# Kernel optimization log

Measured on AMD Instinct MI355X. Metric: run time of the kernel, lower is better.

The kernel has to match this reference:

```python
import jax, jax.numpy as jnp
import numpy as np

B, LH, HF = 65536, 128, 32
VC_MIN = 0.0


def _theta_init():
    # Deterministic parameter init, matching the torch constructor defaults.
    def spinv(x):
        return float(np.log(np.exp(max(x, 1e-4)) - 1.0 + 1e-6))
    vals = [
        0.0,                                  # alpha_raw: log(0.5/(1-0.5))
        float(np.log(np.exp(1.0) - 1.0 + 1e-6)),   # c_raw  (c_init=1.0)
        float(np.log(np.exp(0.1) - 1.0 + 1e-6)),   # kappa_raw (kappa_init=0.1)
        float(np.log(np.exp(0.15) - 1.0 + 1e-6)),  # vc_raw (vc_eff=0.15)
        -6.0,   # log_qx
        -6.0,   # log_qu
        -5.0,   # log_r
        0.0,    # log_q_scale
        -6.0,   # log_p0_xx
        -4.0,   # log_p0_uu
        spinv(0.1),   # a1_raw
        spinv(0.05),  # d1_raw
        spinv(0.5),   # d2_raw
        spinv(0.5),   # d3_raw
        0.0,    # b1
        0.0,    # b2
        0.1,    # beta
        float(np.arctanh(0.9)),  # rho_m_raw
        -4.0,   # log_qm
        -4.0,   # log_p0_mm
    ]
    return np.asarray(vals, dtype=np.float32)


def setup_inputs() -> dict:
    key = jax.random.key(0)
    k1, k2, k3, k4, k5 = jax.random.split(key, 5)
    return {
        "v_hist": jax.random.normal(k1, (B, LH), dtype=jnp.float32),
        "dt_hist": 0.01 + 0.1 * jax.random.uniform(k2, (B, LH), dtype=jnp.float32),
        "x_obs_hist": jax.random.normal(k3, (B, LH), dtype=jnp.float32),
        "v_fut": jax.random.normal(k4, (B, HF), dtype=jnp.float32),
        "dt_fut": 0.01 + 0.1 * jax.random.uniform(k5, (B, HF), dtype=jnp.float32),
        "theta": jnp.asarray(_theta_init()),
    }


def _forward(v_hist, dt_hist, x_obs_hist, v_fut, dt_fut, theta):
    sp = jax.nn.softplus
    alpha = jax.nn.sigmoid(theta[0])
    c = sp(theta[1]); kappa = sp(theta[2]); vc = sp(theta[3]) + VC_MIN
    qx = jnp.exp(theta[4]); qu = jnp.exp(theta[5]); R = jnp.exp(theta[6])
    qs = jnp.exp(theta[7]); p0xx = jnp.exp(theta[8]); p0uu = jnp.exp(theta[9])
    a1 = sp(theta[10]); d1 = sp(theta[11]); d2 = sp(theta[12]); d3 = sp(theta[13])
    b1 = theta[14]; b2 = theta[15]; beta = theta[16]
    rho_m = jnp.tanh(theta[17]); qm = jnp.exp(theta[18]); p0mm = jnp.exp(theta[19])

    Bn, Lh = v_hist.shape
    dtype = v_hist.dtype
    eye = jnp.eye(3, dtype=dtype)

    def predict(s, P, v, dv, dt):
        x, u, m = s[:, 0], s[:, 1], s[:, 2]
        rho = jnp.exp(-alpha * dt)
        forcing = jax.nn.relu(v * v - vc * vc)
        cl = (-a1 * u + b1 * v + b2 * dv
              - d1 * u * u - d2 * u * jnp.abs(v) - d3 * u * jnp.abs(u))
        x_p = x + u * dt
        u_p = rho * u - kappa * x * dt + c * forcing * dt + cl * dt + beta * m
        m_p = rho_m * m
        s_p = jnp.stack([x_p, u_p, m_p], axis=1)
        z = jnp.zeros_like(dt); o = jnp.ones_like(dt)
        Fm = jnp.stack([
            jnp.stack([o, dt, z], axis=1),
            jnp.stack([-kappa * dt, rho, beta * o], axis=1),
            jnp.stack([z, z, rho_m * o], axis=1)], axis=1)  # [B,3,3]
        qdiag = jnp.stack([qs * qx * dt, qs * qu * dt, qm * o], axis=1)  # [B,3]
        P_p = jnp.einsum('bij,bjk,blk->bil', Fm, P, Fm) + qdiag[:, :, None] * eye
        return s_p, P_p

    def update(s, P, y):
        innov = y - s[:, 0]
        S = P[:, 0, 0] + R
        K = P[:, :, 0] / S[:, None]            # [B,3]
        s_u = s + K * innov[:, None]
        IKH = eye - K[:, :, None] * eye[0]     # I - K H, H = [1,0,0]
        P_u = (jnp.einsum('bij,bjk,blk->bil', IKH, P, IKH)
               + R * (K[:, :, None] * K[:, None, :]))
        return s_u, P_u

    s0 = jnp.zeros((Bn, 3), dtype).at[:, 0].set(x_obs_hist[:, 0])
    P0 = jnp.broadcast_to(jnp.diag(jnp.stack([p0xx, p0uu, p0mm])).astype(dtype),
                          (Bn, 3, 3))

    # History steps k = 1 .. Lh-1 (scan over time axis, [T, B] layout)
    v_h = v_hist[:, :Lh - 1].T
    dv_h = jnp.concatenate(
        [jnp.zeros((1, Bn), dtype), (v_hist[:, 1:Lh - 1] - v_hist[:, :Lh - 2]).T], axis=0)
    dt_h = jnp.maximum(dt_hist[:, 1:], 1e-6).T
    y_h = x_obs_hist[:, 1:].T

    def hist_step(carry, inp):
        s, P = carry
        v, dv, dt, y = inp
        s, P = predict(s, P, v, dv, dt)
        s, P = update(s, P, y)
        return (s, P), None

    (s, P), _ = jax.lax.scan(hist_step, (s0, P0), (v_h, dv_h, dt_h, y_h))

    # Future rollout (predict only)
    v_f = v_fut.T
    dv_f = (v_fut - jnp.concatenate([v_hist[:, -1:], v_fut[:, :-1]], axis=1)).T
    dt_f = jnp.maximum(dt_fut, 1e-6).T

    def fut_step(carry, inp):
        s, P = carry
        v, dv, dt = inp
        s, P = predict(s, P, v, dv, dt)
        return (s, P), (s[:, 0], P[:, 0, 0], s[:, 1])

    _, (x_preds, x_vars, u_ests) = jax.lax.scan(fut_step, (s, P), (v_f, dv_f, dt_f))
    return x_preds.T, x_vars.T, u_ests.T  # each [B, Hf]


def reference(v_hist, dt_hist, x_obs_hist, v_fut, dt_fut, theta):
    return _forward(v_hist, dt_hist, x_obs_hist, v_fut, dt_fut, theta)
```

## Files before the change

### kernel.cpp

```cpp
#include <hip/hip_runtime.h>
#include <math.h>

#define BATCH 65536
#define LHIST 128
#define HFUT  32

__device__ __forceinline__ float softplusf(float x) {
    return fmaxf(x, 0.0f) + log1pf(expf(-fabsf(x)));
}

#define KSLOT(buf, st, c, row) ((((((buf)*16 + (st))*3 + (c))*256)) + (row))

__global__ __launch_bounds__(512, 2) void kalman_fwd(
    const float* __restrict__ v_hist,
    const float* __restrict__ dt_hist,
    const float* __restrict__ x_obs,
    const float* __restrict__ v_fut,
    const float* __restrict__ dt_fut,
    const float* __restrict__ theta,
    float* __restrict__ out)
{
    const int tid = threadIdx.x;
    const bool isP = (tid < 256);
    const int row  = tid & 255;
    const int b    = blockIdx.x * 256 + row;

    __shared__ float Kls[2 * 16 * 3 * 256];

    const float alpha = 1.0f / (1.0f + expf(-theta[0]));
    const float c     = softplusf(theta[1]);
    const float kappa = softplusf(theta[2]);
    const float vc    = softplusf(theta[3]);
    const float qx    = expf(theta[4]);
    const float qu    = expf(theta[5]);
    const float Rn    = expf(theta[6]);
    const float qs    = expf(theta[7]);
    const float p0xx  = expf(theta[8]);
    const float p0uu  = expf(theta[9]);
    const float a1    = softplusf(theta[10]);
    const float d1    = softplusf(theta[11]);
    const float d2    = softplusf(theta[12]);
    const float d3    = softplusf(theta[13]);
    const float b1    = theta[14];
    const float b2    = theta[15];
    const float beta  = theta[16];
    const float rho_m = tanhf(theta[17]);
    const float qm    = expf(theta[18]);
    const float p0mm  = expf(theta[19]);
    const float vc2   = vc * vc;
    const float qxs   = qs * qx;
    const float qus   = qs * qu;
    const float rm2   = rho_m * rho_m;
    const float nal2e = -alpha * 1.44269504088896340736f;

    float p00 = p0xx, p01 = 0.0f, p02 = 0.0f, p11 = p0uu, p12 = 0.0f, p22 = p0mm;
    float sx = 0.0f, su = 0.0f, sm = 0.0f, vp1 = 0.0f, vp2 = 0.0f;

    auto P_step = [&](float dt_raw, int buf, int st) {
        float dt  = fmaxf(dt_raw, 1e-6f);
        float rho = __builtin_amdgcn_exp2f(nal2e * dt);
        float kdt = kappa * dt;
        float f0 = p00 + dt * p01;
        float f1 = p01 + dt * p11;
        float f2 = p02 + dt * p12;
        float g0 = -kdt * p00 + rho * p01 + beta * p02;
        float g1 = -kdt * p01 + rho * p11 + beta * p12;
        float g2 = -kdt * p02 + rho * p12 + beta * p22;
        float n00 = f0 + dt * f1 + qxs * dt;
        float n01 = -kdt * f0 + rho * f1 + beta * f2;
        float n02 = rho_m * f2;
        float n11 = -kdt * g0 + rho * g1 + beta * g2 + qus * dt;
        float n12 = rho_m * g2;
        float n22 = rm2 * p22 + qm;
        float S    = n00 + Rn;
        float Sinv = __builtin_amdgcn_rcpf(S);
        float K0 = n00 * Sinv, K1 = n01 * Sinv, K2 = n02 * Sinv;
        Kls[KSLOT(buf, st, 0, row)] = K0;
        Kls[KSLOT(buf, st, 1, row)] = K1;
        Kls[KSLOT(buf, st, 2, row)] = K2;
        float a = 1.0f - K0;
        p00 = a * a * n00 + Rn * K0 * K0;
        p01 = a * (n01 - K1 * n00) + Rn * K0 * K1;
        p02 = a * (n02 - K2 * n00) + Rn * K0 * K2;
        p11 = S * K1 * K1 - 2.0f * K1 * n01 + n11;
        p12 = S * K1 * K2 - K2 * n01 - K1 * n02 + n12;
        p22 = S * K2 * K2 - 2.0f * K2 * n02 + n22;
    };

    auto P_pred = [&](float dt_raw) {
        float dt  = fmaxf(dt_raw, 1e-6f);
        float rho = __builtin_amdgcn_exp2f(nal2e * dt);
        float kdt = kappa * dt;
        float f0 = p00 + dt * p01;
        float f1 = p01 + dt * p11;
        float f2 = p02 + dt * p12;
        float g0 = -kdt * p00 + rho * p01 + beta * p02;
        float g1 = -kdt * p01 + rho * p11 + beta * p12;
        float g2 = -kdt * p02 + rho * p12 + beta * p22;
        float n00 = f0 + dt * f1 + qxs * dt;
        float n01 = -kdt * f0 + rho * f1 + beta * f2;
        float n02 = rho_m * f2;
        float n11 = -kdt * g0 + rho * g1 + beta * g2 + qus * dt;
        float n12 = rho_m * g2;
        float n22 = rm2 * p22 + qm;
        p00 = n00; p01 = n01; p02 = n02; p11 = n11; p12 = n12; p22 = n22;
    };

    auto s_pred = [&](float v, float dv, float dt_raw) {
        float dt  = fmaxf(dt_raw, 1e-6f);
        float rho = __builtin_amdgcn_exp2f(nal2e * dt);
        float forcing = fmaxf(v * v - vc2, 0.0f);
        float cl = -a1 * su + b1 * v + b2 * dv
                 - d1 * su * su - d2 * su * fabsf(v) - d3 * su * fabsf(su);
        float kdt = kappa * dt;
        float x_p = sx + su * dt;
        float u_p = rho * su - kdt * sx + c * forcing * dt + cl * dt + beta * sm;
        float m_p = rho_m * sm;
        sx = x_p; su = u_p; sm = m_p;
    };

    auto s_step = [&](float vnew, float dt_raw, float y, int buf, int st) {
        float K0 = Kls[KSLOT(buf, st, 0, row)];
        float K1 = Kls[KSLOT(buf, st, 1, row)];
        float K2 = Kls[KSLOT(buf, st, 2, row)];
        s_pred(vp1, vp1 - vp2, dt_raw);
        float innov = y - sx;
        sx += K0 * innov; su += K1 * innov; sm += K2 * innov;
        vp2 = vp1; vp1 = vnew;
    };

    const float4* v4 = (const float4*)(v_hist  + (size_t)b * LHIST);
    const float4* d4 = (const float4*)(dt_hist + (size_t)b * LHIST);
    const float4* y4 = (const float4*)(x_obs   + (size_t)b * LHIST);

    {
        if (isP) {
            float cdt[16];
            float4* C = (float4*)cdt;
            #pragma unroll
            for (int i = 0; i < 4; ++i) C[i] = d4[i];
            #pragma unroll
            for (int st = 1; st < 16; ++st) P_step(cdt[st], 0, st);
        }
        __syncthreads();

        #pragma unroll 1
        for (int k = 1; k < 8; ++k) {
            if (isP) {
                float cdt[16];
                float4* C = (float4*)cdt;
                #pragma unroll
                for (int i = 0; i < 4; ++i) C[i] = d4[k * 4 + i];
                int buf = k & 1;
                P_step(cdt[0], buf, 0);
                #pragma unroll
                for (int st = 1; st < 16; ++st) P_step(cdt[st], buf, st);
            } else {
                int j = k - 1;
                float cv[16], cd[16], cy[16];
                float4* V = (float4*)cv; float4* D = (float4*)cd; float4* Y = (float4*)cy;
                #pragma unroll
                for (int i = 0; i < 4; ++i) {
                    V[i] = v4[j * 4 + i]; D[i] = d4[j * 4 + i]; Y[i] = y4[j * 4 + i];
                }
                int buf = j & 1;
                if (j == 0) {
                    sx = cy[0]; vp1 = cv[0]; vp2 = cv[0];
                } else {
                    s_step(cv[0], cd[0], cy[0], buf, 0);
                }
                #pragma unroll
                for (int st = 1; st < 16; ++st) s_step(cv[st], cd[st], cy[st], buf, st);
            }
            __syncthreads();
        }

        if (!isP) {
            const int j = 7;
            float cv[16], cd[16], cy[16];
            float4* V = (float4*)cv; float4* D = (float4*)cd; float4* Y = (float4*)cy;
            #pragma unroll
            for (int i = 0; i < 4; ++i) {
                V[i] = v4[j * 4 + i]; D[i] = d4[j * 4 + i]; Y[i] = y4[j * 4 + i];
            }
            s_step(cv[0], cd[0], cy[0], 1, 0);
            #pragma unroll
            for (int st = 1; st < 16; ++st) s_step(cv[st], cd[st], cy[st], 1, st);
        }
    }

    if (isP) {
        float fdt[32];
        float4* FD = (float4*)fdt;
        const float4* df4 = (const float4*)(dt_fut + (size_t)b * HFUT);
        #pragma unroll
        for (int i = 0; i < 8; ++i) FD[i] = df4[i];
        float oxv[32];
        #pragma unroll
        for (int j = 0; j < HFUT; ++j) { P_pred(fdt[j]); oxv[j] = p00; }
        float4* xv = (float4*)(out + (size_t)BATCH * HFUT + (size_t)b * HFUT);
        float4* OXV = (float4*)oxv;
        #pragma unroll
        for (int i = 0; i < 8; ++i) xv[i] = OXV[i];
    } else {
        float fv[32], fdt[32];
        float4* FV = (float4*)fv; float4* FD = (float4*)fdt;
        const float4* vf4 = (const float4*)(v_fut  + (size_t)b * HFUT);
        const float4* df4 = (const float4*)(dt_fut + (size_t)b * HFUT);
        #pragma unroll
        for (int i = 0; i < 8; ++i) { FV[i] = vf4[i]; FD[i] = df4[i]; }
        float oxp[32], oue[32];
        float vp = vp1;
        #pragma unroll
        for (int j = 0; j < HFUT; ++j) {
            s_pred(fv[j], fv[j] - vp, fdt[j]);
            vp = fv[j];
            oxp[j] = sx; oue[j] = su;
        }
        float4* xp = (float4*)(out + (size_t)b * HFUT);
        float4* ue = (float4*)(out + 2 * (size_t)BATCH * HFUT + (size_t)b * HFUT);
        float4* OXP = (float4*)oxp; float4* OUE = (float4*)oue;
        #pragma unroll
        for (int i = 0; i < 8; ++i) { xp[i] = OXP[i]; ue[i] = OUE[i]; }
    }
}

extern "C" void kernel_launch(void* const* d_in, const int* in_sizes, int n_in,
                              void* d_out, int out_size, void* d_ws, size_t ws_size,
                              hipStream_t stream) {
    const float* v_hist  = (const float*)d_in[0];
    const float* dt_hist = (const float*)d_in[1];
    const float* x_obs   = (const float*)d_in[2];
    const float* v_fut   = (const float*)d_in[3];
    const float* dt_fut  = (const float*)d_in[4];
    const float* theta   = (const float*)d_in[5];
    float* out = (float*)d_out;

    dim3 grid(BATCH / 256), block(512);
    hipLaunchKernelGGL(kalman_fwd, grid, block, 0, stream,
                       v_hist, dt_hist, x_obs, v_fut, dt_fut, theta, out);
}
```

Before: 179.6 us.

## Software-pipeline chunk loads with double-buffered registers across producer/consumer phases

Unrolls the history loop into explicit phases where each warp group prefetches the next 16-step chunk of inputs into a second register buffer while it computes on the current one. This is meant to hide global-memory load latency behind the serial Kalman recurrence instead of stalling at the start of each chunk. The cost is higher register pressure from the doubled input buffers, which under launch_bounds(512,2) could cause spills.

New measurement: 204.3 us. 1.14x slower.

```diff
diff --git a/kernel.cpp b/kernel.cpp
--- a/kernel.cpp
+++ b/kernel.cpp
@@ -9,7 +9,7 @@
     return fmaxf(x, 0.0f) + log1pf(expf(-fabsf(x)));
 }
 
-#define KSLOT(buf, st, c, row) ((((((buf)*16 + (st))*3 + (c))*256)) + (row))
+#define KSLOT(buf, st, c, row) (((((buf)*16 + (st))*3 + (c))*256) + (row))
 
 __global__ __launch_bounds__(512, 2) void kalman_fwd(
     const float* __restrict__ v_hist,
@@ -133,76 +133,96 @@
     const float4* d4 = (const float4*)(dt_hist + (size_t)b * LHIST);
     const float4* y4 = (const float4*)(x_obs   + (size_t)b * LHIST);
 
-    {
-        if (isP) {
-            float cdt[16];
-            float4* C = (float4*)cdt;
-            #pragma unroll
-            for (int i = 0; i < 4; ++i) C[i] = d4[i];
-            #pragma unroll
-            for (int st = 1; st < 16; ++st) P_step(cdt[st], 0, st);
-        }
-        __syncthreads();
-
-        #pragma unroll 1
-        for (int k = 1; k < 8; ++k) {
-            if (isP) {
-                float cdt[16];
-                float4* C = (float4*)cdt;
-                #pragma unroll
-                for (int i = 0; i < 4; ++i) C[i] = d4[k * 4 + i];
-                int buf = k & 1;
-                P_step(cdt[0], buf, 0);
-                #pragma unroll
-                for (int st = 1; st < 16; ++st) P_step(cdt[st], buf, st);
-            } else {
-                int j = k - 1;
-                float cv[16], cd[16], cy[16];
-                float4* V = (float4*)cv; float4* D = (float4*)cd; float4* Y = (float4*)cy;
-                #pragma unroll
-                for (int i = 0; i < 4; ++i) {
-                    V[i] = v4[j * 4 + i]; D[i] = d4[j * 4 + i]; Y[i] = y4[j * 4 + i];
-                }
-                int buf = j & 1;
-                if (j == 0) {
-                    sx = cy[0]; vp1 = cv[0]; vp2 = cv[0];
-                } else {
-                    s_step(cv[0], cd[0], cy[0], buf, 0);
-                }
-                #pragma unroll
-                for (int st = 1; st < 16; ++st) s_step(cv[st], cd[st], cy[st], buf, st);
-            }
-            __syncthreads();
-        }
-
-        if (!isP) {
-            const int j = 7;
-            float cv[16], cd[16], cy[16];
-            float4* V = (float4*)cv; float4* D = (float4*)cd; float4* Y = (float4*)cy;
-            #pragma unroll
-            for (int i = 0; i < 4; ++i) {
-                V[i] = v4[j * 4 + i]; D[i] = d4[j * 4 + i]; Y[i] = y4[j * 4 + i];
-            }
-            s_step(cv[0], cd[0], cy[0], 1, 0);
-            #pragma unroll
-            for (int st = 1; st < 16; ++st) s_step(cv[st], cd[st], cy[st], 1, st);
-        }
-    }
-
-    if (isP) {
-        float fdt[32];
-        float4* FD = (float4*)fdt;
+    auto ld16 = [&](float (&dst)[16], const float4* src, int g) {
+        float4* D = (float4*)dst;
+        #pragma unroll
+        for (int i = 0; i < 4; ++i) D[i] = src[g * 4 + i];
+    };
+
+    auto P_cons = [&](const float (&dtc)[16], int buf) {
+        #pragma unroll
+        for (int st = 0; st < 16; ++st) P_step(dtc[st], buf, st);
+    };
+    auto s_cons = [&](const float (&vv)[16], const float (&dd)[16],
+                      const float (&yy)[16], int buf) {
+        #pragma unroll
+        for (int st = 0; st < 16; ++st) s_step(vv[st], dd[st], yy[st], buf, st);
+    };
+
+    float pA[16], pB[16];
+    float sva[16], sda[16], sya[16];
+    float svb[16], sdb[16], syb[16];
+    float fdtP[32];
+
+
+    if (isP) {
+        ld16(pA, d4, 0); ld16(pB, d4, 1);
+        #pragma unroll
+        for (int st = 1; st < 16; ++st) P_step(pA[st], 0, st);
+        ld16(pA, d4, 2);
+    } else {
+        ld16(sva, v4, 0); ld16(sda, d4, 0); ld16(sya, y4, 0);
+        ld16(svb, v4, 1); ld16(sdb, d4, 1); ld16(syb, y4, 1);
+    }
+    __syncthreads();
+
+    if (isP) {
+        P_cons(pB, 1);
+        ld16(pB, d4, 3);
+    } else {
+        sx = sya[0]; vp1 = sva[0]; vp2 = sva[0];
+        #pragma unroll
+        for (int st = 1; st < 16; ++st) s_step(sva[st], sda[st], sya[st], 0, st);
+        ld16(sva, v4, 2); ld16(sda, d4, 2); ld16(sya, y4, 2);
+    }
+    __syncthreads();
+
+    if (isP) { P_cons(pA, 0); ld16(pA, d4, 4); }
+    else     { s_cons(svb, sdb, syb, 1);
+               ld16(svb, v4, 3); ld16(sdb, d4, 3); ld16(syb, y4, 3); }
+    __syncthreads();
+
+    if (isP) { P_cons(pB, 1); ld16(pB, d4, 5); }
+    else     { s_cons(sva, sda, sya, 0);
+               ld16(sva, v4, 4); ld16(sda, d4, 4); ld16(sya, y4, 4); }
+    __syncthreads();
+
+    if (isP) { P_cons(pA, 0); ld16(pA, d4, 6); }
+    else     { s_cons(svb, sdb, syb, 1);
+               ld16(svb, v4, 5); ld16(sdb, d4, 5); ld16(syb, y4, 5); }
+    __syncthreads();
+
+    if (isP) { P_cons(pB, 1); ld16(pB, d4, 7); }
+    else     { s_cons(sva, sda, sya, 0);
+               ld16(sva, v4, 6); ld16(sda, d4, 6); ld16(sya, y4, 6); }
+    __syncthreads();
+
+    if (isP) {
+        P_cons(pA, 0);
+        float4* FD = (float4*)fdtP;
         const float4* df4 = (const float4*)(dt_fut + (size_t)b * HFUT);
         #pragma unroll
         for (int i = 0; i < 8; ++i) FD[i] = df4[i];
+    } else {
+        s_cons(svb, sdb, syb, 1);
+        ld16(svb, v4, 7); ld16(sdb, d4, 7); ld16(syb, y4, 7);
+    }
+    __syncthreads();
+
+    if (isP) { P_cons(pB, 1); }
+    else     { s_cons(sva, sda, sya, 0); }
+    __syncthreads();
+
+    if (isP) {
         float oxv[32];
         #pragma unroll
-        for (int j = 0; j < HFUT; ++j) { P_pred(fdt[j]); oxv[j] = p00; }
+        for (int j = 0; j < HFUT; ++j) { P_pred(fdtP[j]); oxv[j] = p00; }
         float4* xv = (float4*)(out + (size_t)BATCH * HFUT + (size_t)b * HFUT);
         float4* OXV = (float4*)oxv;
         #pragma unroll
         for (int i = 0; i < 8; ++i) xv[i] = OXV[i];
     } else {
+        s_cons(svb, sdb, syb, 1);
         float fv[32], fdt[32];
         float4* FV = (float4*)fv; float4* FD = (float4*)fdt;
         const float4* vf4 = (const float4*)(v_fut  + (size_t)b * HFUT);
```

## Shrink blocks to one P-wave and one s-wave with register prefetch ring

Applied to the files above, without the earlier changes.

Shrinks each block to 128 threads covering 64 batch rows, one wavefront doing the covariance/gain recursion and one doing the state recursion. Work is split into 8-step chunks in a double-buffered shared ring, and each wave prefetches the next chunk of inputs into registers while computing the current one. The P-wave also writes dt and rho to the ring, so the state wave no longer reads dt_hist or evaluates exp2. The aim is to hide global-load latency, keep barriers between just two waves, and remove repeated transcendental work, at the cost of more barriers per step and more blocks to schedule.

Result: faster. 171.9 us (-4.2%).

```diff
diff --git a/kernel.cpp b/kernel.cpp
--- a/kernel.cpp
+++ b/kernel.cpp
@@ -4,14 +4,15 @@
 #define BATCH 65536
 #define LHIST 128
 #define HFUT  32
+#define NR    64
 
 __device__ __forceinline__ float softplusf(float x) {
     return fmaxf(x, 0.0f) + log1pf(expf(-fabsf(x)));
 }
 
-#define KSLOT(buf, st, c, row) ((((((buf)*16 + (st))*3 + (c))*256)) + (row))
-
-__global__ __launch_bounds__(512, 2) void kalman_fwd(
+#define RS(buf, st, c) ((((buf)*8 + (st))*5 + (c))*NR)
+
+__global__ __launch_bounds__(128, 2) void kalman_fwd(
     const float* __restrict__ v_hist,
     const float* __restrict__ dt_hist,
     const float* __restrict__ x_obs,
@@ -20,12 +21,12 @@
     const float* __restrict__ theta,
     float* __restrict__ out)
 {
-    const int tid = threadIdx.x;
-    const bool isP = (tid < 256);
-    const int row  = tid & 255;
-    const int b    = blockIdx.x * 256 + row;
-
-    __shared__ float Kls[2 * 16 * 3 * 256];
+    const int tid  = threadIdx.x;
+    const int lane = tid & 63;
+    const bool isP = (tid < 64);
+    const int b    = blockIdx.x * NR + lane;
+
+    __shared__ float ring[2 * 8 * 5 * NR];
 
     const float alpha = 1.0f / (1.0f + expf(-theta[0]));
     const float c     = softplusf(theta[1]);
@@ -75,9 +76,11 @@
         float S    = n00 + Rn;
         float Sinv = __builtin_amdgcn_rcpf(S);
         float K0 = n00 * Sinv, K1 = n01 * Sinv, K2 = n02 * Sinv;
-        Kls[KSLOT(buf, st, 0, row)] = K0;
-        Kls[KSLOT(buf, st, 1, row)] = K1;
-        Kls[KSLOT(buf, st, 2, row)] = K2;
+        ring[RS(buf, st, 0) + lane] = K0;
+        ring[RS(buf, st, 1) + lane] = K1;
+        ring[RS(buf, st, 2) + lane] = K2;
+        ring[RS(buf, st, 3) + lane] = dt;
+        ring[RS(buf, st, 4) + lane] = rho;
         float a = 1.0f - K0;
         p00 = a * a * n00 + Rn * K0 * K0;
         p01 = a * (n01 - K1 * n00) + Rn * K0 * K1;
@@ -106,6 +109,25 @@
         p00 = n00; p01 = n01; p02 = n02; p11 = n11; p12 = n12; p22 = n22;
     };
 
+    auto s_step = [&](float vnew, float y, int buf, int st) {
+        float K0  = ring[RS(buf, st, 0) + lane];
+        float K1  = ring[RS(buf, st, 1) + lane];
+        float K2  = ring[RS(buf, st, 2) + lane];
+        float dt  = ring[RS(buf, st, 3) + lane];
+        float rho = ring[RS(buf, st, 4) + lane];
+        float v = vp1, dv = vp1 - vp2;
+        float forcing = fmaxf(v * v - vc2, 0.0f);
+        float cl = -a1 * su + b1 * v + b2 * dv
+                 - d1 * su * su - d2 * su * fabsf(v) - d3 * su * fabsf(su);
+        float x_p = sx + su * dt;
+        float u_p = rho * su - (kappa * dt) * sx + c * forcing * dt + cl * dt + beta * sm;
+        float m_p = rho_m * sm;
+        sx = x_p; su = u_p; sm = m_p;
+        float innov = y - sx;
+        sx += K0 * innov; su += K1 * innov; sm += K2 * innov;
+        vp2 = vp1; vp1 = vnew;
+    };
+
     auto s_pred = [&](float v, float dv, float dt_raw) {
         float dt  = fmaxf(dt_raw, 1e-6f);
         float rho = __builtin_amdgcn_exp2f(nal2e * dt);
@@ -119,90 +141,84 @@
         sx = x_p; su = u_p; sm = m_p;
     };
 
-    auto s_step = [&](float vnew, float dt_raw, float y, int buf, int st) {
-        float K0 = Kls[KSLOT(buf, st, 0, row)];
-        float K1 = Kls[KSLOT(buf, st, 1, row)];
-        float K2 = Kls[KSLOT(buf, st, 2, row)];
-        s_pred(vp1, vp1 - vp2, dt_raw);
-        float innov = y - sx;
-        sx += K0 * innov; su += K1 * innov; sm += K2 * innov;
-        vp2 = vp1; vp1 = vnew;
-    };
-
     const float4* v4 = (const float4*)(v_hist  + (size_t)b * LHIST);
     const float4* d4 = (const float4*)(dt_hist + (size_t)b * LHIST);
     const float4* y4 = (const float4*)(x_obs   + (size_t)b * LHIST);
 
-    {
+    auto ld8 = [&](float (&dst)[8], const float4* src, int chunk) {
+        float4* D = (float4*)dst;
+        D[0] = src[chunk * 2]; D[1] = src[chunk * 2 + 1];
+    };
+
+    float dtA[8], dtB[8];
+    float vA[8], yA[8], vB[8], yB[8];
+
+    if (isP) { ld8(dtA, d4, 0); ld8(dtB, d4, 1); }
+    else     { ld8(vA, v4, 0); ld8(yA, y4, 0); ld8(vB, v4, 1); ld8(yB, y4, 1); }
+
+    if (isP) {
+        #pragma unroll
+        for (int st = 1; st < 8; ++st) P_step(dtA[st], 0, st);
+        ld8(dtA, d4, 2);
+    }
+    __syncthreads();
+
+    #pragma unroll 1
+    for (int it = 0; it < 7; ++it) {
         if (isP) {
-            float cdt[16];
-            float4* C = (float4*)cdt;
             #pragma unroll
-            for (int i = 0; i < 4; ++i) C[i] = d4[i];
-            #pragma unroll
-            for (int st = 1; st < 16; ++st) P_step(cdt[st], 0, st);
+            for (int st = 0; st < 8; ++st) P_step(dtB[st], 1, st);
+            ld8(dtB, d4, 2 * it + 3);
+        } else {
+            if (it == 0) {
+                sx = yA[0]; vp1 = vA[0]; vp2 = vA[0];
+                #pragma unroll
+                for (int st = 1; st < 8; ++st) s_step(vA[st], yA[st], 0, st);
+            } else {
+                #pragma unroll
+                for (int st = 0; st < 8; ++st) s_step(vA[st], yA[st], 0, st);
+            }
+            ld8(vA, v4, 2 * it + 2); ld8(yA, y4, 2 * it + 2);
         }
         __syncthreads();
-
-        #pragma unroll 1
-        for (int k = 1; k < 8; ++k) {
-            if (isP) {
-                float cdt[16];
-                float4* C = (float4*)cdt;
-                #pragma unroll
-                for (int i = 0; i < 4; ++i) C[i] = d4[k * 4 + i];
-                int buf = k & 1;
-                P_step(cdt[0], buf, 0);
-                #pragma unroll
-                for (int st = 1; st < 16; ++st) P_step(cdt[st], buf, st);
-            } else {
-                int j = k - 1;
-                float cv[16], cd[16], cy[16];
-                float4* V = (float4*)cv; float4* D = (float4*)cd; float4* Y = (float4*)cy;
-                #pragma unroll
-                for (int i = 0; i < 4; ++i) {
-                    V[i] = v4[j * 4 + i]; D[i] = d4[j * 4 + i]; Y[i] = y4[j * 4 + i];
-                }
-                int buf = j & 1;
-                if (j == 0) {
-                    sx = cy[0]; vp1 = cv[0]; vp2 = cv[0];
-                } else {
-                    s_step(cv[0], cd[0], cy[0], buf, 0);
-                }
-                #pragma unroll
-                for (int st = 1; st < 16; ++st) s_step(cv[st], cd[st], cy[st], buf, st);
-            }
-            __syncthreads();
+        if (isP) {
+            #pragma unroll
+            for (int st = 0; st < 8; ++st) P_step(dtA[st], 0, st);
+            int nc = 2 * it + 4; nc = (nc > 15) ? 15 : nc;
+            ld8(dtA, d4, nc);
+        } else {
+            #pragma unroll
+            for (int st = 0; st < 8; ++st) s_step(vB[st], yB[st], 1, st);
+            ld8(vB, v4, 2 * it + 3); ld8(yB, y4, 2 * it + 3);
         }
-
-        if (!isP) {
-            const int j = 7;
-            float cv[16], cd[16], cy[16];
-            float4* V = (float4*)cv; float4* D = (float4*)cd; float4* Y = (float4*)cy;
-            #pragma unroll
-            for (int i = 0; i < 4; ++i) {
-                V[i] = v4[j * 4 + i]; D[i] = d4[j * 4 + i]; Y[i] = y4[j * 4 + i];
-            }
-            s_step(cv[0], cd[0], cy[0], 1, 0);
-            #pragma unroll
-            for (int st = 1; st < 16; ++st) s_step(cv[st], cd[st], cy[st], 1, st);
-        }
-    }
-
+        __syncthreads();
+    }
+
+    float fdtP[32];
     if (isP) {
-        float fdt[32];
-        float4* FD = (float4*)fdt;
+        #pragma unroll
+        for (int st = 0; st < 8; ++st) P_step(dtB[st], 1, st);
+        float4* FD = (float4*)fdtP;
         const float4* df4 = (const float4*)(dt_fut + (size_t)b * HFUT);
         #pragma unroll
         for (int i = 0; i < 8; ++i) FD[i] = df4[i];
+    } else {
+        #pragma unroll
+        for (int st = 0; st < 8; ++st) s_step(vA[st], yA[st], 0, st);
+    }
+    __syncthreads();
+
+    if (isP) {
         float oxv[32];
         #pragma unroll
-        for (int j = 0; j < HFUT; ++j) { P_pred(fdt[j]); oxv[j] = p00; }
+        for (int j = 0; j < HFUT; ++j) { P_pred(fdtP[j]); oxv[j] = p00; }
         float4* xv = (float4*)(out + (size_t)BATCH * HFUT + (size_t)b * HFUT);
         float4* OXV = (float4*)oxv;
         #pragma unroll
         for (int i = 0; i < 8; ++i) xv[i] = OXV[i];
     } else {
+        #pragma unroll
+        for (int st = 0; st < 8; ++st) s_step(vB[st], yB[st], 1, st);
         float fv[32], fdt[32];
         float4* FV = (float4*)fv; float4* FD = (float4*)fdt;
         const float4* vf4 = (const float4*)(v_fut  + (size_t)b * HFUT);
@@ -236,7 +252,7 @@
     const float* theta   = (const float*)d_in[5];
     float* out = (float*)d_out;
 
-    dim3 grid(BATCH / 256), block(512);
+    dim3 grid(BATCH / NR), block(128);
     hipLaunchKernelGGL(kalman_fwd, grid, block, 0, stream,
                        v_hist, dt_hist, x_obs, v_fut, dt_fut, theta, out);
 }
```
